# Kernel tuning notes

Measured on AMD Instinct MI355X. Metric: run time of the kernel, lower is better.

Reference implementation:

```python
import jax, jax.numpy as jnp
import numpy as np

B, H, W, C, HEADS = 8, 64, 64, 128, 4
H_SP, W_SP = 64, 8            # idx=0: H_sp = H, W_sp = split_size
HD = C // HEADS               # 32
N = H_SP * W_SP               # 512 tokens per window
SCALE = HD ** -0.5


def setup_inputs() -> dict:
    key = jax.random.key(0)
    k1, k2, k3 = jax.random.split(key, 3)
    return {
        "qkv": jax.random.normal(k1, (3, B, H * W, C), dtype=jnp.float32),
        "conv_w": jax.random.normal(k2, (C, 1, 3, 3), dtype=jnp.float32) * 0.1,
        "conv_b": jax.random.normal(k3, (C,), dtype=jnp.float32) * 0.1,
    }


def _to_windows(x):
    # x: [B, L, C] -> window tokens [Bw, N, C] with Bw = B * (H//H_SP) * (W//W_SP)
    x = x.reshape(B, H // H_SP, H_SP, W // W_SP, W_SP, C)
    x = x.transpose(0, 1, 3, 2, 4, 5).reshape(-1, N, C)
    return x


def _heads(x):
    # [Bw, N, C] -> [Bw, heads, N, hd]
    return x.reshape(-1, N, HEADS, HD).transpose(0, 2, 1, 3)


def reference(qkv, conv_w, conv_b):
    q, k, v = qkv[0], qkv[1], qkv[2]

    qw = _heads(_to_windows(q)) * SCALE   # [Bw, h, N, hd]
    kw = _heads(_to_windows(k))

    vwin = _to_windows(v)                 # [Bw, N, C]
    # LePE: depthwise 3x3 conv on each window (NHWC, feature_group_count=C)
    vimg = vwin.reshape(-1, H_SP, W_SP, C)
    w_hwio = conv_w.transpose(2, 3, 1, 0)  # [3,3,1,C]
    lepe = jax.lax.conv_general_dilated(
        vimg, w_hwio, window_strides=(1, 1), padding='SAME',
        dimension_numbers=('NHWC', 'HWIO', 'NHWC'), feature_group_count=C,
    ) + conv_b
    lepe = _heads(lepe.reshape(-1, N, C))  # [Bw, h, N, hd]
    vw = _heads(vwin)

    attn = jax.nn.softmax(jnp.einsum('whqd,whkd->whqk', qw, kw), axis=-1)
    out = jnp.einsum('whqk,whkd->whqd', attn, vw) + lepe  # [Bw, h, N, hd]

    # merge heads and windows back to [B, L, C]
    out = out.transpose(0, 2, 1, 3).reshape(-1, N, C)
    out = out.reshape(B, H // H_SP, W // W_SP, H_SP, W_SP, C)
    out = out.transpose(0, 1, 3, 2, 4, 5).reshape(B, H * W, C)
    return out
```

## Files before the change

### kernel.cpp

```cpp
#include <hip/hip_runtime.h>


namespace {
constexpr int Bn   = 8;
constexpr int Ww   = 64;
constexpr int Cc   = 128;
constexpr int HD   = 32;
constexpr int WSP  = 8;
constexpr int NTOK = 512;
constexpr int LL   = 64 * 64;
constexpr float SCALE_L2E = 0.17677669529663687f * 1.4426950408889634f;
constexpr int KPAD = 40;
constexpr int VPAD = 536;
}

typedef __bf16 bf16x8 __attribute__((ext_vector_type(8)));
typedef float  f32x16 __attribute__((ext_vector_type(16)));
typedef unsigned int uint32x4 __attribute__((ext_vector_type(4)));

__device__ inline unsigned cvtpk(float x, float y) {
    unsigned r;
    asm("v_cvt_pk_bf16_f32 %0, %1, %2" : "=v"(r) : "v"(x), "v"(y));
    return r;
}

__global__ __launch_bounds__(1024, 4) void attn_kernel(const float* __restrict__ qkv,
                                                       const float* __restrict__ cw,
                                                       const float* __restrict__ cb,
                                                       float* __restrict__ out) {
    const int blk = blockIdx.x;
    const int w   = blk >> 2;
    const int h   = blk & 3;
    const int b   = w >> 3;
    const int wb  = w & 7;
    const int tid = threadIdx.x;
    const int wv  = tid >> 6;
    const int lane = tid & 63;
    const int l31 = lane & 31;
    const int h5  = lane >> 5;

    const float* qp = qkv;
    const float* kp = qkv + (size_t)Bn * LL * Cc;
    const float* vp = qkv + (size_t)2 * Bn * LL * Cc;

    __shared__ short K_lds[NTOK][KPAD];
    __shared__ short VT_lds[HD][VPAD];

    const int tpa = tid >> 3,          ja = tid & 7;
    const int tpb = (tid + 1024) >> 3, jb = (tid + 1024) & 7;
    const int t0a = tpa * 2, t0b = tpb * 2;
    const int lqa = (t0a >> 3) * Ww + wb * WSP + (t0a & 7);
    const int lqb = (t0b >> 3) * Ww + wb * WSP + (t0b & 7);
    const size_t ga = ((size_t)b * LL + lqa) * Cc + h * HD + ja * 4;
    const size_t gb = ((size_t)b * LL + lqb) * Cc + h * HD + jb * 4;
    const float4 k0a = *reinterpret_cast<const float4*>(kp + ga);
    const float4 k1a = *reinterpret_cast<const float4*>(kp + ga + Cc);
    const float4 v0a = *reinterpret_cast<const float4*>(vp + ga);
    const float4 v1a = *reinterpret_cast<const float4*>(vp + ga + Cc);
    const float4 k0b = *reinterpret_cast<const float4*>(kp + gb);
    const float4 k1b = *reinterpret_cast<const float4*>(kp + gb + Cc);
    const float4 v0b = *reinterpret_cast<const float4*>(vp + gb);
    const float4 v1b = *reinterpret_cast<const float4*>(vp + gb + Cc);

    const int qtok = wv * 32 + l31;
    const int qlqi = (qtok >> 3) * Ww + wb * WSP + (qtok & 7);
    const float* qptr = qp + ((size_t)b * LL + qlqi) * Cc + h * HD + h5 * 8;
    const float4 qa0 = *reinterpret_cast<const float4*>(qptr);
    const float4 qc0 = *reinterpret_cast<const float4*>(qptr + 4);
    const float4 qa1 = *reinterpret_cast<const float4*>(qptr + 16);
    const float4 qc1 = *reinterpret_cast<const float4*>(qptr + 20);

    {
        uint2 pk0, pk1;
        pk0.x = cvtpk(k0a.x, k0a.y);  pk0.y = cvtpk(k0a.z, k0a.w);
        pk1.x = cvtpk(k1a.x, k1a.y);  pk1.y = cvtpk(k1a.z, k1a.w);
        *reinterpret_cast<uint2*>(&K_lds[t0a][ja * 4]) = pk0;
        *reinterpret_cast<uint2*>(&K_lds[t0a + 1][ja * 4]) = pk1;
        *reinterpret_cast<unsigned*>(&VT_lds[ja * 4 + 0][t0a]) = cvtpk(v0a.x, v1a.x);
        *reinterpret_cast<unsigned*>(&VT_lds[ja * 4 + 1][t0a]) = cvtpk(v0a.y, v1a.y);
        *reinterpret_cast<unsigned*>(&VT_lds[ja * 4 + 2][t0a]) = cvtpk(v0a.z, v1a.z);
        *reinterpret_cast<unsigned*>(&VT_lds[ja * 4 + 3][t0a]) = cvtpk(v0a.w, v1a.w);
    }
    {
        uint2 pk0, pk1;
        pk0.x = cvtpk(k0b.x, k0b.y);  pk0.y = cvtpk(k0b.z, k0b.w);
        pk1.x = cvtpk(k1b.x, k1b.y);  pk1.y = cvtpk(k1b.z, k1b.w);
        *reinterpret_cast<uint2*>(&K_lds[t0b][jb * 4]) = pk0;
        *reinterpret_cast<uint2*>(&K_lds[t0b + 1][jb * 4]) = pk1;
        *reinterpret_cast<unsigned*>(&VT_lds[jb * 4 + 0][t0b]) = cvtpk(v0b.x, v1b.x);
        *reinterpret_cast<unsigned*>(&VT_lds[jb * 4 + 1][t0b]) = cvtpk(v0b.y, v1b.y);
        *reinterpret_cast<unsigned*>(&VT_lds[jb * 4 + 2][t0b]) = cvtpk(v0b.z, v1b.z);
        *reinterpret_cast<unsigned*>(&VT_lds[jb * 4 + 3][t0b]) = cvtpk(v0b.w, v1b.w);
    }

    bf16x8 qf[2];
    {
        uint32x4 u;
        u.x = cvtpk(qa0.x * SCALE_L2E, qa0.y * SCALE_L2E);
        u.y = cvtpk(qa0.z * SCALE_L2E, qa0.w * SCALE_L2E);
        u.z = cvtpk(qc0.x * SCALE_L2E, qc0.y * SCALE_L2E);
        u.w = cvtpk(qc0.z * SCALE_L2E, qc0.w * SCALE_L2E);
        qf[0] = __builtin_bit_cast(bf16x8, u);
        u.x = cvtpk(qa1.x * SCALE_L2E, qa1.y * SCALE_L2E);
        u.y = cvtpk(qa1.z * SCALE_L2E, qa1.w * SCALE_L2E);
        u.z = cvtpk(qc1.x * SCALE_L2E, qc1.y * SCALE_L2E);
        u.w = cvtpk(qc1.z * SCALE_L2E, qc1.w * SCALE_L2E);
        qf[1] = __builtin_bit_cast(bf16x8, u);
    }
    __syncthreads();

    f32x16 acc  = (f32x16)(0.f);
    f32x16 lacc = (f32x16)(0.f);
    const f32x16 z16 = (f32x16)(0.f);

    uint32x4 onesu;
    onesu.x = 0x3F803F80u; onesu.y = 0x3F803F80u;
    onesu.z = 0x3F803F80u; onesu.w = 0x3F803F80u;
    const bf16x8 onesf = __builtin_bit_cast(bf16x8, onesu);

    auto load_kf = [&](int kt, bf16x8* kf) {
        const int krow = kt * 32 + l31;
#pragma unroll
        for (int dc = 0; dc < 2; ++dc)
            kf[dc] = __builtin_bit_cast(bf16x8,
                *reinterpret_cast<const uint32x4*>(&K_lds[krow][dc * 16 + h5 * 8]));
    };

    bf16x8 kf[2];
    load_kf(0, kf);

    for (int kt = 0; kt < 16; ++kt) {
        f32x16 s = z16;
        s = __builtin_amdgcn_mfma_f32_32x32x16_bf16(kf[0], qf[0], s, 0, 0, 0);
        s = __builtin_amdgcn_mfma_f32_32x32x16_bf16(kf[1], qf[1], s, 0, 0, 0);

        bf16x8 kfn[2];
        load_kf((kt + 1) & 15, kfn);
        uint32x4 vu[2];
#pragma unroll
        for (int kw = 0; kw < 2; ++kw) {
            const int kcol = kt * 32 + kw * 16 + h5 * 8;
            vu[kw] = *reinterpret_cast<const uint32x4*>(&VT_lds[l31][kcol]);
        }

        float pe[16];
#pragma unroll
        for (int i = 0; i < 16; ++i) pe[i] = __builtin_amdgcn_exp2f(s[i]);
        unsigned dw[8];
#pragma unroll
        for (int i = 0; i < 8; ++i) dw[i] = cvtpk(pe[2 * i], pe[2 * i + 1]);

#pragma unroll
        for (int kw = 0; kw < 2; ++kw) {
            unsigned a0 = dw[4 * kw + 0], b0 = dw[4 * kw + 2];
            unsigned a1 = dw[4 * kw + 1], b1 = dw[4 * kw + 3];
            asm("v_permlane32_swap_b32 %0, %1" : "+v"(a0), "+v"(b0));
            asm("v_permlane32_swap_b32 %0, %1" : "+v"(a1), "+v"(b1));
            uint32x4 pu; pu.x = a0; pu.y = a1; pu.z = b0; pu.w = b1;
            const bf16x8 pf = __builtin_bit_cast(bf16x8, pu);
            acc  = __builtin_amdgcn_mfma_f32_32x32x16_bf16(
                pf, __builtin_bit_cast(bf16x8, vu[kw]), acc, 0, 0, 0);
            lacc = __builtin_amdgcn_mfma_f32_32x32x16_bf16(
                pf, onesf, lacc, 0, 0, 0);
        }
        kf[0] = kfn[0];
        kf[1] = kfn[1];
    }

    const int ch = h * HD + l31;
    float wreg[9];
#pragma unroll
    for (int wi = 0; wi < 9; ++wi) wreg[wi] = cw[ch * 9 + wi];
    const float bias = cb[ch];

    const int tok0 = wv * 32;
    unsigned hw[26];
    {
        const int segbase = tok0 + 4 * h5 - 12;
#pragma unroll
        for (int c2 = 0; c2 < 13; ++c2) {
            int t = segbase + 4 * c2;
            t = t < 0 ? 0 : (t > NTOK - 4 ? NTOK - 4 : t);
            const uint2 u = *reinterpret_cast<const uint2*>(&VT_lds[l31][t]);
            hw[c2 * 2 + 0] = u.x;
            hw[c2 * 2 + 1] = u.y;
        }
    }

#pragma unroll
    for (int r = 0; r < 16; ++r) {
        const int c_r = (r & 3) + 8 * (r >> 2);
        const float iv = __builtin_amdgcn_rcpf(lacc[r]);
        const int tok = tok0 + c_r + 4 * h5;
        float cv = bias;
#pragma unroll
        for (int dy = -1; dy <= 1; ++dy) {
            const bool rowok = (unsigned)(tok + dy * 8) < (unsigned)NTOK;
#pragma unroll
            for (int dx = -1; dx <= 1; ++dx) {
                const int idx = c_r + 12 + dy * 8 + dx;
                const unsigned word = hw[idx >> 1];
                const float tap = __builtin_bit_cast(float,
                    (idx & 1) ? (word & 0xFFFF0000u) : (word << 16));
                bool ok = rowok;
                if (dx == -1) ok = ok && (((r & 3) != 0) || (h5 != 0));
                if (dx == +1) ok = ok && (((r & 3) != 3) || (h5 == 0));
                cv += ok ? wreg[(dy + 1) * 3 + (dx + 1)] * tap : 0.f;
            }
        }
        const int lqi = (tok >> 3) * Ww + wb * WSP + (tok & 7);
        out[((size_t)b * LL + lqi) * Cc + ch] = acc[r] * iv + cv;
    }
}

extern "C" void kernel_launch(void* const* d_in, const int* in_sizes, int n_in,
                              void* d_out, int out_size, void* d_ws, size_t ws_size,
                              hipStream_t stream) {
    const float* qkv = (const float*)d_in[0];
    const float* cw  = (const float*)d_in[1];
    const float* cb  = (const float*)d_in[2];
    float* out = (float*)d_out;

    attn_kernel<<<256, 1024, 0, stream>>>(qkv, cw, cb, out);
}
```

Baseline: 28.74 us.

## Split KV staging into two halves to overlap second-half stores with first-half attention

The kernel now stages only the first 256 tokens of K and V into LDS before the first sync, runs attention over those 8 key tiles, then converts and stores the second half (already loaded into registers and pinned by an empty asm) before a second barrier and the remaining 8 tiles. The goal is to hide the global load latency and LDS store work for the second half behind the first half's MFMA and exp work. It adds a second block-wide barrier and keeps 16 extra float registers live across the first phase, which may pressure registers under the 1024-thread launch bound.

```diff
diff --git a/kernel.cpp b/kernel.cpp
--- a/kernel.cpp
+++ b/kernel.cpp
@@ -16,6 +16,7 @@
 
 typedef __bf16 bf16x8 __attribute__((ext_vector_type(8)));
 typedef float  f32x16 __attribute__((ext_vector_type(16)));
+typedef float  fx4    __attribute__((ext_vector_type(4)));
 typedef unsigned int uint32x4 __attribute__((ext_vector_type(4)));
 
 __device__ inline unsigned cvtpk(float x, float y) {
@@ -46,21 +47,23 @@
     __shared__ short K_lds[NTOK][KPAD];
     __shared__ short VT_lds[HD][VPAD];
 
-    const int tpa = tid >> 3,          ja = tid & 7;
-    const int tpb = (tid + 1024) >> 3, jb = (tid + 1024) & 7;
-    const int t0a = tpa * 2, t0b = tpb * 2;
+    const int ja  = tid & 7;
+    const int t0a = (tid >> 3) * 2;
+    const int t0b = ((tid + 1024) >> 3) * 2;
     const int lqa = (t0a >> 3) * Ww + wb * WSP + (t0a & 7);
     const int lqb = (t0b >> 3) * Ww + wb * WSP + (t0b & 7);
     const size_t ga = ((size_t)b * LL + lqa) * Cc + h * HD + ja * 4;
-    const size_t gb = ((size_t)b * LL + lqb) * Cc + h * HD + jb * 4;
-    const float4 k0a = *reinterpret_cast<const float4*>(kp + ga);
-    const float4 k1a = *reinterpret_cast<const float4*>(kp + ga + Cc);
-    const float4 v0a = *reinterpret_cast<const float4*>(vp + ga);
-    const float4 v1a = *reinterpret_cast<const float4*>(vp + ga + Cc);
-    const float4 k0b = *reinterpret_cast<const float4*>(kp + gb);
-    const float4 k1b = *reinterpret_cast<const float4*>(kp + gb + Cc);
-    const float4 v0b = *reinterpret_cast<const float4*>(vp + gb);
-    const float4 v1b = *reinterpret_cast<const float4*>(vp + gb + Cc);
+    const size_t gb = ((size_t)b * LL + lqb) * Cc + h * HD + ja * 4;
+
+    const float4 kA0 = *reinterpret_cast<const float4*>(kp + ga);
+    const float4 kA1 = *reinterpret_cast<const float4*>(kp + ga + Cc);
+    const float4 vA0 = *reinterpret_cast<const float4*>(vp + ga);
+    const float4 vA1 = *reinterpret_cast<const float4*>(vp + ga + Cc);
+    fx4 kB0 = *reinterpret_cast<const fx4*>(kp + gb);
+    fx4 kB1 = *reinterpret_cast<const fx4*>(kp + gb + Cc);
+    fx4 vB0 = *reinterpret_cast<const fx4*>(vp + gb);
+    fx4 vB1 = *reinterpret_cast<const fx4*>(vp + gb + Cc);
+    asm volatile("" : "+v"(kB0), "+v"(kB1), "+v"(vB0), "+v"(vB1));
 
     const int qtok = wv * 32 + l31;
     const int qlqi = (qtok >> 3) * Ww + wb * WSP + (qtok & 7);
@@ -72,25 +75,14 @@
 
     {
         uint2 pk0, pk1;
-        pk0.x = cvtpk(k0a.x, k0a.y);  pk0.y = cvtpk(k0a.z, k0a.w);
-        pk1.x = cvtpk(k1a.x, k1a.y);  pk1.y = cvtpk(k1a.z, k1a.w);
+        pk0.x = cvtpk(kA0.x, kA0.y);  pk0.y = cvtpk(kA0.z, kA0.w);
+        pk1.x = cvtpk(kA1.x, kA1.y);  pk1.y = cvtpk(kA1.z, kA1.w);
         *reinterpret_cast<uint2*>(&K_lds[t0a][ja * 4]) = pk0;
         *reinterpret_cast<uint2*>(&K_lds[t0a + 1][ja * 4]) = pk1;
-        *reinterpret_cast<unsigned*>(&VT_lds[ja * 4 + 0][t0a]) = cvtpk(v0a.x, v1a.x);
-        *reinterpret_cast<unsigned*>(&VT_lds[ja * 4 + 1][t0a]) = cvtpk(v0a.y, v1a.y);
-        *reinterpret_cast<unsigned*>(&VT_lds[ja * 4 + 2][t0a]) = cvtpk(v0a.z, v1a.z);
-        *reinterpret_cast<unsigned*>(&VT_lds[ja * 4 + 3][t0a]) = cvtpk(v0a.w, v1a.w);
-    }
-    {
-        uint2 pk0, pk1;
-        pk0.x = cvtpk(k0b.x, k0b.y);  pk0.y = cvtpk(k0b.z, k0b.w);
-        pk1.x = cvtpk(k1b.x, k1b.y);  pk1.y = cvtpk(k1b.z, k1b.w);
-        *reinterpret_cast<uint2*>(&K_lds[t0b][jb * 4]) = pk0;
-        *reinterpret_cast<uint2*>(&K_lds[t0b + 1][jb * 4]) = pk1;
-        *reinterpret_cast<unsigned*>(&VT_lds[jb * 4 + 0][t0b]) = cvtpk(v0b.x, v1b.x);
-        *reinterpret_cast<unsigned*>(&VT_lds[jb * 4 + 1][t0b]) = cvtpk(v0b.y, v1b.y);
-        *reinterpret_cast<unsigned*>(&VT_lds[jb * 4 + 2][t0b]) = cvtpk(v0b.z, v1b.z);
-        *reinterpret_cast<unsigned*>(&VT_lds[jb * 4 + 3][t0b]) = cvtpk(v0b.w, v1b.w);
+        *reinterpret_cast<unsigned*>(&VT_lds[ja * 4 + 0][t0a]) = cvtpk(vA0.x, vA1.x);
+        *reinterpret_cast<unsigned*>(&VT_lds[ja * 4 + 1][t0a]) = cvtpk(vA0.y, vA1.y);
+        *reinterpret_cast<unsigned*>(&VT_lds[ja * 4 + 2][t0a]) = cvtpk(vA0.z, vA1.z);
+        *reinterpret_cast<unsigned*>(&VT_lds[ja * 4 + 3][t0a]) = cvtpk(vA0.w, vA1.w);
     }
 
     bf16x8 qf[2];
@@ -125,31 +117,20 @@
             kf[dc] = __builtin_bit_cast(bf16x8,
                 *reinterpret_cast<const uint32x4*>(&K_lds[krow][dc * 16 + h5 * 8]));
     };
-
-    bf16x8 kf[2];
-    load_kf(0, kf);
-
-    for (int kt = 0; kt < 16; ++kt) {
-        f32x16 s = z16;
-        s = __builtin_amdgcn_mfma_f32_32x32x16_bf16(kf[0], qf[0], s, 0, 0, 0);
-        s = __builtin_amdgcn_mfma_f32_32x32x16_bf16(kf[1], qf[1], s, 0, 0, 0);
-
-        bf16x8 kfn[2];
-        load_kf((kt + 1) & 15, kfn);
-        uint32x4 vu[2];
+    auto load_vu = [&](int kt, uint32x4* vu) {
 #pragma unroll
         for (int kw = 0; kw < 2; ++kw) {
             const int kcol = kt * 32 + kw * 16 + h5 * 8;
             vu[kw] = *reinterpret_cast<const uint32x4*>(&VT_lds[l31][kcol]);
         }
-
+    };
+    auto softmax_pv = [&](const f32x16& s, const uint32x4* vu) {
         float pe[16];
 #pragma unroll
         for (int i = 0; i < 16; ++i) pe[i] = __builtin_amdgcn_exp2f(s[i]);
         unsigned dw[8];
 #pragma unroll
         for (int i = 0; i < 8; ++i) dw[i] = cvtpk(pe[2 * i], pe[2 * i + 1]);
-
 #pragma unroll
         for (int kw = 0; kw < 2; ++kw) {
             unsigned a0 = dw[4 * kw + 0], b0 = dw[4 * kw + 2];
@@ -163,9 +144,40 @@
             lacc = __builtin_amdgcn_mfma_f32_32x32x16_bf16(
                 pf, onesf, lacc, 0, 0, 0);
         }
-        kf[0] = kfn[0];
-        kf[1] = kfn[1];
-    }
+    };
+    auto phase = [&](int base) {
+        bf16x8 kf[2];
+        load_kf(base, kf);
+        for (int kt = base; kt < base + 8; ++kt) {
+            f32x16 s = z16;
+            s = __builtin_amdgcn_mfma_f32_32x32x16_bf16(kf[0], qf[0], s, 0, 0, 0);
+            s = __builtin_amdgcn_mfma_f32_32x32x16_bf16(kf[1], qf[1], s, 0, 0, 0);
+            bf16x8 kfn[2];
+            load_kf(base + ((kt + 1 - base) & 7), kfn);
+            uint32x4 vu[2];
+            load_vu(kt, vu);
+            softmax_pv(s, vu);
+            kf[0] = kfn[0];
+            kf[1] = kfn[1];
+        }
+    };
+
+    phase(0);
+
+    {
+        uint2 pk0, pk1;
+        pk0.x = cvtpk(kB0[0], kB0[1]);  pk0.y = cvtpk(kB0[2], kB0[3]);
+        pk1.x = cvtpk(kB1[0], kB1[1]);  pk1.y = cvtpk(kB1[2], kB1[3]);
+        *reinterpret_cast<uint2*>(&K_lds[t0b][ja * 4]) = pk0;
+        *reinterpret_cast<uint2*>(&K_lds[t0b + 1][ja * 4]) = pk1;
+        *reinterpret_cast<unsigned*>(&VT_lds[ja * 4 + 0][t0b]) = cvtpk(vB0[0], vB1[0]);
+        *reinterpret_cast<unsigned*>(&VT_lds[ja * 4 + 1][t0b]) = cvtpk(vB0[1], vB1[1]);
+        *reinterpret_cast<unsigned*>(&VT_lds[ja * 4 + 2][t0b]) = cvtpk(vB0[2], vB1[2]);
+        *reinterpret_cast<unsigned*>(&VT_lds[ja * 4 + 3][t0b]) = cvtpk(vB0[3], vB1[3]);
+    }
+    __syncthreads();
+
+    phase(8);
 
     const int ch = h * HD + l31;
     float wreg[9];
```

Result: slower. 41.45 us (+44.2%).
